# Kernel tuning notes

Measured on AMD Instinct MI355X. Metric: run time of the kernel, lower is better.

The kernel has to match this reference:

```python
import jax, jax.numpy as jnp
import numpy as np

N = 50000
F_IN = 256
F_OUT = 256
K = 5
E = 1_600_000
SQRT_2PI = float(np.sqrt(2.0 * np.pi))
SQRT_2 = float(np.sqrt(2.0))


def _ex_relu(mu, sigma):
    # expected value of relu(Normal(mu, sigma)) with sigma = variance
    is_zero = sigma == 0
    safe_sigma = jnp.where(is_zero, 1e-10, sigma)
    sqrt_sigma = jnp.sqrt(safe_sigma)
    w = mu / sqrt_sigma
    nr = sqrt_sigma * (jnp.exp(-0.5 * w * w) / SQRT_2PI
                       + 0.5 * w * (1.0 + jax.lax.erf(w / SQRT_2)))
    return jnp.where(is_zero, jnp.maximum(mu, 0.0), nr)


def _conv(h, src, dst):
    # SimpleConv(aggr='add', combine_root='self_loop'):
    # out[d] = h[d] + sum_{(s,d) in edges} h[s];  h: [K, N, O]
    agg = jnp.zeros_like(h).at[:, dst, :].add(h[:, src, :])
    return h + agg


def setup_inputs() -> dict:
    key = jax.random.key(0)
    ks = jax.random.split(key, 7)
    x = jax.random.normal(ks[0], (N, F_IN), dtype=jnp.float32)
    edges = jax.random.randint(ks[1], (2, E), 0, N, dtype=jnp.int64)
    mask = jax.random.randint(ks[2], (N, F_IN), 0, 2) == 1  # True = missing
    logp = jax.random.normal(ks[3], (K,), dtype=jnp.float32)
    means = jax.random.normal(ks[4], (K, F_IN), dtype=jnp.float32)
    logvars = jax.random.normal(ks[5], (K, F_IN), dtype=jnp.float32)
    weight = jax.random.normal(ks[6], (F_IN, F_OUT), dtype=jnp.float32) * (1.414 / np.sqrt(F_IN + F_OUT) * np.sqrt(6.0))
    bias = jnp.zeros((F_OUT,), dtype=jnp.float32)
    return {"x": x, "edges": edges, "mask": mask, "logp": logp,
            "means": means, "logvars": logvars, "weight": weight, "bias": bias}


def reference(x, edges, mask, logp, means, logvars, weight, bias):
    src, dst = edges[0], edges[1]
    variances = jnp.exp(logvars)                                   # [K, F]
    m = mask[None, :, :]                                           # [1, N, F]
    mean_mat = jnp.where(m, means[:, None, :], x[None, :, :])      # [K, N, F]
    var_mat = jnp.where(m, variances[:, None, :], 0.0)             # [K, N, F]

    transform_x = jnp.einsum('knf,fo->kno', mean_mat, weight) + bias
    transform_covs = jnp.einsum('knf,fo->kno', var_mat, weight * weight)

    conv_x = _conv(transform_x, src, dst)                          # [K, N, O]
    conv_covs = _conv(transform_covs, src, dst)                    # [K, N, O]

    expected_x = _ex_relu(conv_x, conv_covs)                       # [K, N, O]

    # GMM responsibilities over components
    diff2 = (mean_mat - means[:, None, :]) ** 2 / variances[:, None, :]
    log_n = (-0.5 * jnp.sum(diff2, axis=2)
             - 0.5 * F_IN * np.log(2.0 * np.pi)
             - 0.5 * jnp.sum(logvars))                             # [K, N]
    gamma = jax.nn.softmax(logp[:, None] + log_n, axis=0)          # [K, N]

    return jnp.sum(expected_x * gamma[:, :, None], axis=0)         # [N, O]
```

## Files before the change

### kernel.cpp

```cpp
#include <hip/hip_runtime.h>
#include <math.h>

#define F 256
#define KMIX 5
#define RECB 640
#define GR 16
#define GS 3136

typedef __attribute__((ext_vector_type(8))) short bf16x8;
typedef __attribute__((ext_vector_type(4))) float f32x4;

__device__ __forceinline__ float bf2f(unsigned short u) {
  union { unsigned int i; float f; } v; v.i = ((unsigned int)u) << 16; return v.f;
}
__device__ __forceinline__ unsigned short f2bf(float f) {
  union { float f; unsigned int i; } v; v.f = f;
  unsigned int u = v.i;
  unsigned int r = (u + 0x7fffu + ((u >> 16) & 1u)) >> 16;
  return (unsigned short)r;
}

__device__ __forceinline__ f32x4 MFMA(bf16x8 a, bf16x8 b, f32x4 c) {
  return __builtin_amdgcn_mfma_f32_16x16x32_bf16(a, b, c, 0, 0, 0);
}

__device__ __forceinline__ float ex_relu_fast(float mu, float sig) {
  const float c1 = 1.2732395447f;
  const float c2 = 2.5464790895f;
  float t = mu * mu;
  float u = t + c1 * sig;
  float v = t + c2 * sig + 1e-20f;
  float r = __builtin_amdgcn_rsqf(v);
  return 0.5f * mu + 0.5f * u * r;
}

__global__ void kzero(unsigned int* p, long long n) {
  long long i = (long long)blockIdx.x * blockDim.x + threadIdx.x;
  long long stride = (long long)gridDim.x * blockDim.x;
  for (; i < n; i += stride) p[i] = 0u;
}

__global__ __launch_bounds__(256) void k_tab(const float* __restrict__ logvars,
                                             float* __restrict__ ivar) {
  int i = blockIdx.x * 256 + threadIdx.x;
  if (i < KMIX * F) ivar[i] = __expf(-logvars[i]);
}

__global__ __launch_bounds__(256) void k_prep(
    const float* __restrict__ x, const int* __restrict__ mask,
    const float* __restrict__ logp, const float* __restrict__ means,
    const float* __restrict__ ivar,
    unsigned char* __restrict__ rec, float* __restrict__ gamma, int Npad) {
  int n = blockIdx.x;
  int f = threadIdx.x;
  int idx = n * F + f;
  float xv = x[idx];
  int m = mask[idx];
  unsigned char* rn = rec + (size_t)n * RECB;
  ((unsigned short*)rn)[f] = m ? (unsigned short)0 : f2bf(xv);
  int wave = threadIdx.x >> 6;
  int lane = threadIdx.x & 63;
  unsigned long long bal = __ballot(m != 0);
  if (lane == 0) *(unsigned long long*)(rn + 512 + wave * 8) = bal;
  float cb[KMIX];
#pragma unroll
  for (int k = 0; k < KMIX; ++k) {
    float d = xv - means[k * F + f];
    cb[k] = m ? 0.0f : d * d * ivar[k * F + f];
  }
  __shared__ float red[KMIX][4];
#pragma unroll
  for (int k = 0; k < KMIX; ++k) {
    float c = cb[k];
    for (int off = 32; off > 0; off >>= 1) c += __shfl_down(c, off, 64);
    if (lane == 0) red[k][wave] = c;
  }
  __syncthreads();
  if (threadIdx.x == 0) {
    float lg[KMIX], mx = -1e30f;
#pragma unroll
    for (int k = 0; k < KMIX; ++k) {
      float tot = red[k][0] + red[k][1] + red[k][2] + red[k][3];
      lg[k] = logp[k] - 0.5f * tot;
      mx = fmaxf(mx, lg[k]);
    }
    float den = 0.0f, e[KMIX];
#pragma unroll
    for (int k = 0; k < KMIX; ++k) { e[k] = __expf(lg[k] - mx); den += e[k]; }
    float inv = 1.0f / den;
#pragma unroll
    for (int k = 0; k < KMIX; ++k) gamma[k * Npad + n] = e[k] * inv;
  }
}

__global__ void k_count(const int* __restrict__ edges, int* __restrict__ cnt, int E) {
  int i = blockIdx.x * blockDim.x + threadIdx.x;
  if (i < E) {
    int dst = edges[E + i];
    int g = edges[i] / GS;
    atomicAdd(&cnt[dst * GR + g], 1);
  }
}

__global__ __launch_bounds__(1024) void k_scanA(const int* __restrict__ cnt,
                                                int* __restrict__ excl,
                                                int* __restrict__ bsum, int n) {
  __shared__ int s[1024];
  int t = threadIdx.x;
  int i = blockIdx.x * 1024 + t;
  int v = (i < n) ? cnt[i] : 0;
  s[t] = v;
  __syncthreads();
  for (int off = 1; off < 1024; off <<= 1) {
    int u = (t >= off) ? s[t - off] : 0;
    __syncthreads();
    s[t] += u;
    __syncthreads();
  }
  if (i < n) excl[i] = s[t] - v;
  if (t == 1023) bsum[blockIdx.x] = s[1023];
}

__global__ __launch_bounds__(1024) void k_scanB(int* __restrict__ bsum, int nb) {
  __shared__ int s[1024];
  int t = threadIdx.x;
  int v = (t < nb) ? bsum[t] : 0;
  s[t] = v;
  __syncthreads();
  for (int off = 1; off < 1024; off <<= 1) {
    int u = (t >= off) ? s[t - off] : 0;
    __syncthreads();
    s[t] += u;
    __syncthreads();
  }
  if (t < nb) bsum[t] = s[t] - v;
}

__global__ __launch_bounds__(1024) void k_scanC(int* __restrict__ offs,
                                                int* __restrict__ cur,
                                                const int* __restrict__ bsum,
                                                int n, int E) {
  int i = blockIdx.x * 1024 + threadIdx.x;
  if (i < n) {
    int v = offs[i] + bsum[blockIdx.x];
    offs[i] = v;
    cur[i] = v;
  }
  if (i == 0) offs[n] = E;
}

__global__ void k_fill(const int* __restrict__ edges, int* __restrict__ cur,
                       int* __restrict__ srclist, int E) {
  int i = blockIdx.x * blockDim.x + threadIdx.x;
  if (i < E) {
    int src = edges[i];
    int dst = edges[E + i];
    int g = src / GS;
    int pos = atomicAdd(&cur[dst * GR + g], 1);
    srclist[pos] = src;
  }
}

__global__ __launch_bounds__(1024) void k_gather(
    const unsigned char* __restrict__ rec,
    const int* __restrict__ offs, const int* __restrict__ srclist,
    unsigned short* __restrict__ xs_pack, unsigned short* __restrict__ sm_pack,
    float* __restrict__ degp1) {
  __shared__ float xs_l[16][257];
  __shared__ float sm_l[16][257];
  int tile = blockIdx.x;
  int wave = threadIdx.x >> 6, lane = threadIdx.x & 63;
  int fb = lane * 4;
  int n = tile * 16 + wave;
  const unsigned char* rn = rec + (size_t)n * RECB;
  ushort4 xv = *(const ushort4*)(rn + lane * 8);
  unsigned int mw = *(const unsigned int*)(rn + 512 + ((lane >> 3) << 2));
  unsigned int nib = (mw >> ((lane & 7) * 4)) & 0xFu;
  unsigned int macc = (nib | (nib << 7) | (nib << 14) | (nib << 21)) & 0x01010101u;
  float a0 = bf2f(xv.x), a1 = bf2f(xv.y), a2 = bf2f(xv.z), a3 = bf2f(xv.w);
  int s0 = offs[n * GR], s1 = offs[n * GR + GR];
  int i = s0;
  for (; i + 4 <= s1; i += 4) {
    int sa = srclist[i], sb = srclist[i + 1], sc = srclist[i + 2], sd = srclist[i + 3];
    const unsigned char* ra = rec + (size_t)sa * RECB;
    const unsigned char* rb = rec + (size_t)sb * RECB;
    const unsigned char* rc = rec + (size_t)sc * RECB;
    const unsigned char* rd = rec + (size_t)sd * RECB;
    ushort4 va = *(const ushort4*)(ra + lane * 8);
    ushort4 vb = *(const ushort4*)(rb + lane * 8);
    ushort4 vc = *(const ushort4*)(rc + lane * 8);
    ushort4 vd = *(const ushort4*)(rd + lane * 8);
    unsigned int wa = *(const unsigned int*)(ra + 512 + ((lane >> 3) << 2));
    unsigned int wb = *(const unsigned int*)(rb + 512 + ((lane >> 3) << 2));
    unsigned int wc = *(const unsigned int*)(rc + 512 + ((lane >> 3) << 2));
    unsigned int wd = *(const unsigned int*)(rd + 512 + ((lane >> 3) << 2));
    a0 += bf2f(va.x) + bf2f(vb.x) + bf2f(vc.x) + bf2f(vd.x);
    a1 += bf2f(va.y) + bf2f(vb.y) + bf2f(vc.y) + bf2f(vd.y);
    a2 += bf2f(va.z) + bf2f(vb.z) + bf2f(vc.z) + bf2f(vd.z);
    a3 += bf2f(va.w) + bf2f(vb.w) + bf2f(vc.w) + bf2f(vd.w);
    unsigned int na = (wa >> ((lane & 7) * 4)) & 0xFu;
    unsigned int nb = (wb >> ((lane & 7) * 4)) & 0xFu;
    unsigned int nc = (wc >> ((lane & 7) * 4)) & 0xFu;
    unsigned int nd = (wd >> ((lane & 7) * 4)) & 0xFu;
    macc += (na | (na << 7) | (na << 14) | (na << 21)) & 0x01010101u;
    macc += (nb | (nb << 7) | (nb << 14) | (nb << 21)) & 0x01010101u;
    macc += (nc | (nc << 7) | (nc << 14) | (nc << 21)) & 0x01010101u;
    macc += (nd | (nd << 7) | (nd << 14) | (nd << 21)) & 0x01010101u;
  }
  for (; i < s1; ++i) {
    int s = srclist[i];
    const unsigned char* rs = rec + (size_t)s * RECB;
    ushort4 sv = *(const ushort4*)(rs + lane * 8);
    unsigned int ws = *(const unsigned int*)(rs + 512 + ((lane >> 3) << 2));
    a0 += bf2f(sv.x); a1 += bf2f(sv.y); a2 += bf2f(sv.z); a3 += bf2f(sv.w);
    unsigned int ns = (ws >> ((lane & 7) * 4)) & 0xFu;
    macc += (ns | (ns << 7) | (ns << 14) | (ns << 21)) & 0x01010101u;
  }
  xs_l[wave][fb] = a0; xs_l[wave][fb + 1] = a1; xs_l[wave][fb + 2] = a2; xs_l[wave][fb + 3] = a3;
  sm_l[wave][fb] = (float)(macc & 0xFFu);
  sm_l[wave][fb + 1] = (float)((macc >> 8) & 0xFFu);
  sm_l[wave][fb + 2] = (float)((macc >> 16) & 0xFFu);
  sm_l[wave][fb + 3] = (float)(macc >> 24);
  if (lane == 0) degp1[n] = (float)(s1 - s0 + 1);
  __syncthreads();
  if (threadIdx.x < 512) {
    int slot = threadIdx.x;
    int kt = slot >> 6, l = slot & 63;
    int r = l & 15, q = l >> 4;
    int fbase = kt * 32 + q * 8;
    bf16x8 vx, vs;
#pragma unroll
    for (int j = 0; j < 8; ++j) {
      vx[j] = (short)f2bf(xs_l[r][fbase + j]);
      vs[j] = (short)f2bf(sm_l[r][fbase + j]);
    }
    long long po = ((long long)tile * 8 + kt) * 64 + l;
    ((bf16x8*)xs_pack)[po] = vx;
    ((bf16x8*)sm_pack)[po] = vs;
  }
}

__global__ __launch_bounds__(64) void k_bpack(
    const float* __restrict__ weight, const float* __restrict__ means,
    const float* __restrict__ logvars, unsigned short* __restrict__ bpack) {
  int bid = blockIdx.x;
  int kt = bid & 7, ot = (bid >> 3) & 15, m = bid >> 7;
  int l = threadIdx.x;
  int r = l & 15, q = l >> 4;
  int o = ot * 16 + r;
  bf16x8 v;
#pragma unroll
  for (int j = 0; j < 8; ++j) {
    int f = kt * 32 + q * 8 + j;
    float wv = weight[f * F + o];
    float val;
    if (m == 0) val = wv;
    else if (m <= 5) val = means[(m - 1) * F + f] * wv;
    else val = __expf(logvars[(m - 6) * F + f]) * wv * wv;
    v[j] = (short)f2bf(val);
  }
  ((bf16x8*)bpack)[((long long)(m * 16 + ot) * 8 + kt) * 64 + l] = v;
}

__global__ __launch_bounds__(256, 3) void k_gemm(
    const unsigned short* __restrict__ xs_pack, const unsigned short* __restrict__ sm_pack,
    const unsigned short* __restrict__ bpack, const float* __restrict__ degp1,
    const float* __restrict__ gamma, const float* __restrict__ bias,
    float* __restrict__ out, int N, int Npad, int RB) {
  int L = blockIdx.x;
  int rb = (L >> 5) * 8 + (L & 7);
  int bo = (L >> 3) & 3;
  if (rb >= RB) return;
  __shared__ unsigned char sp_lds[32768];
  int tid = threadIdx.x;
  int wave = tid >> 6, lane = tid & 63;
  int rw = wave >> 1, cw = wave & 1;
  int q = lane >> 4, r16 = lane & 15;
  int rt0 = rb * 4 + rw * 2;
  int ct0 = bo * 4 + cw * 2;
  const bf16x8* XP = (const bf16x8*)xs_pack;
  const bf16x8* BP = (const bf16x8*)bpack;

  {
    const uint4* src = (const uint4*)((const unsigned char*)sm_pack + (size_t)rb * 32768) + tid;
    uint4* dst = (uint4*)(void*)sp_lds + tid;
#pragma unroll
    for (int it = 0; it < 8; ++it) dst[it * 256] = src[it * 256];
  }

  f32x4 C1[2][2];
#pragma unroll
  for (int rt = 0; rt < 2; ++rt)
#pragma unroll
    for (int cc = 0; cc < 2; ++cc) C1[rt][cc] = (f32x4){0.f, 0.f, 0.f, 0.f};
#pragma unroll
  for (int kt = 0; kt < 8; ++kt) {
    bf16x8 a0 = XP[((size_t)rt0 * 8 + kt) * 64 + lane];
    bf16x8 a1 = XP[((size_t)(rt0 + 1) * 8 + kt) * 64 + lane];
#pragma unroll
    for (int cc = 0; cc < 2; ++cc) {
      bf16x8 b = BP[((size_t)(ct0 + cc) * 8 + kt) * 64 + lane];
      C1[0][cc] = MFMA(a0, b, C1[0][cc]);
      C1[1][cc] = MFMA(a1, b, C1[1][cc]);
    }
  }

  int row0 = rb * 64 + rw * 32 + q * 4;
  float dp[2][4];
#pragma unroll
  for (int rt = 0; rt < 2; ++rt)
#pragma unroll
    for (int rr = 0; rr < 4; ++rr) dp[rt][rr] = degp1[row0 + rt * 16 + rr];
  float bs[2];
#pragma unroll
  for (int cc = 0; cc < 2; ++cc) bs[cc] = bias[bo * 64 + cw * 32 + cc * 16 + r16];

  f32x4 outa[2][2];
#pragma unroll
  for (int rt = 0; rt < 2; ++rt)
#pragma unroll
    for (int cc = 0; cc < 2; ++cc) outa[rt][cc] = (f32x4){0.f, 0.f, 0.f, 0.f};

  __syncthreads();
  const unsigned char* myl = sp_lds + rw * 16384;

  for (int k = 0; k < KMIX; ++k) {
    float gm[2][4];
#pragma unroll
    for (int rt = 0; rt < 2; ++rt)
#pragma unroll
      for (int rr = 0; rr < 4; ++rr) gm[rt][rr] = gamma[k * Npad + row0 + rt * 16 + rr];
    f32x4 ax[2][2], ac[2][2];
#pragma unroll
    for (int rt = 0; rt < 2; ++rt)
#pragma unroll
      for (int cc = 0; cc < 2; ++cc) {
        ax[rt][cc] = C1[rt][cc];
        ac[rt][cc] = (f32x4){0.f, 0.f, 0.f, 0.f};
      }
#pragma unroll
    for (int kt = 0; kt < 8; ++kt) {
      bf16x8 sp0 = *(const bf16x8*)(myl + kt * 1024 + lane * 16);
      bf16x8 sp1 = *(const bf16x8*)(myl + 8192 + kt * 1024 + lane * 16);
#pragma unroll
      for (int cc = 0; cc < 2; ++cc) {
        int c = ct0 + cc;
        bf16x8 bw = BP[(((size_t)(1 + k) * 16 + c) * 8 + kt) * 64 + lane];
        bf16x8 bv = BP[(((size_t)(6 + k) * 16 + c) * 8 + kt) * 64 + lane];
        ax[0][cc] = MFMA(sp0, bw, ax[0][cc]);
        ax[1][cc] = MFMA(sp1, bw, ax[1][cc]);
        ac[0][cc] = MFMA(sp0, bv, ac[0][cc]);
        ac[1][cc] = MFMA(sp1, bv, ac[1][cc]);
      }
    }
#pragma unroll
    for (int rt = 0; rt < 2; ++rt)
#pragma unroll
      for (int cc = 0; cc < 2; ++cc)
#pragma unroll
        for (int rr = 0; rr < 4; ++rr) {
          float mu = ax[rt][cc][rr] + dp[rt][rr] * bs[cc];
          float e = ex_relu_fast(mu, ac[rt][cc][rr]);
          outa[rt][cc][rr] += gm[rt][rr] * e;
        }
  }

#pragma unroll
  for (int rt = 0; rt < 2; ++rt)
#pragma unroll
    for (int cc = 0; cc < 2; ++cc) {
      int col = bo * 64 + cw * 32 + cc * 16 + r16;
#pragma unroll
      for (int rr = 0; rr < 4; ++rr) {
        int row = row0 + rt * 16 + rr;
        if (row < N) out[(long long)row * F + col] = outa[rt][cc][rr];
      }
    }
}

extern "C" void kernel_launch(void* const* d_in, const int* in_sizes, int n_in,
                              void* d_out, int out_size, void* d_ws, size_t ws_size,
                              hipStream_t stream) {
  const float* x = (const float*)d_in[0];
  const int* edges = (const int*)d_in[1];
  const int* mask = (const int*)d_in[2];
  const float* logp = (const float*)d_in[3];
  const float* means = (const float*)d_in[4];
  const float* logvars = (const float*)d_in[5];
  const float* weight = (const float*)d_in[6];
  const float* bias = (const float*)d_in[7];
  float* out = (float*)d_out;

  int N = in_sizes[0] / F;
  int E = in_sizes[1] / 2;
  int Npad = ((N + 127) / 128) * 128;
  int RB = Npad / 64;
  int NB = N * GR;
  int SB = (NB + 1023) / 1024;

  char* w = (char*)d_ws;
  auto alloc = [&](size_t bytes) {
    char* p = w;
    w += (bytes + 255) & ~(size_t)255;
    return p;
  };
  unsigned char* rec = (unsigned char*)alloc((size_t)N * RECB);
  unsigned short* xsp = (unsigned short*)alloc((size_t)Npad * F * 2);
  unsigned short* smp = (unsigned short*)alloc((size_t)Npad * F * 2);
  unsigned short* bpk = (unsigned short*)alloc((size_t)11 * F * F * 2);
  int* cnt = (int*)alloc((size_t)NB * 4);
  int* offs = (int*)alloc((size_t)(NB + 1) * 4);
  int* cur = (int*)alloc((size_t)NB * 4);
  int* bsum = (int*)alloc((size_t)1024 * 4);
  int* srclist = (int*)alloc((size_t)E * 4);
  float* degp1 = (float*)alloc((size_t)Npad * 4);
  float* gamma = (float*)alloc((size_t)KMIX * Npad * 4);
  float* ivar = (float*)alloc((size_t)KMIX * F * 4);

  kzero<<<782, 256, 0, stream>>>((unsigned int*)cnt, NB);
  k_tab<<<(KMIX * F + 255) / 256, 256, 0, stream>>>(logvars, ivar);
  k_prep<<<N, 256, 0, stream>>>(x, mask, logp, means, ivar, rec, gamma, Npad);
  k_count<<<(E + 255) / 256, 256, 0, stream>>>(edges, cnt, E);
  k_scanA<<<SB, 1024, 0, stream>>>(cnt, offs, bsum, NB);
  k_scanB<<<1, 1024, 0, stream>>>(bsum, SB);
  k_scanC<<<SB, 1024, 0, stream>>>(offs, cur, bsum, NB, E);
  k_fill<<<(E + 255) / 256, 256, 0, stream>>>(edges, cur, srclist, E);
  k_gather<<<N / 16, 1024, 0, stream>>>(rec, offs, srclist, xsp, smp, degp1);
  k_bpack<<<11 * 16 * 8, 64, 0, stream>>>(weight, means, logvars, bpk);
  int NGG = (RB + 7) / 8;
  k_gemm<<<NGG * 32, 256, 0, stream>>>(xsp, smp, bpk, degp1, gamma, bias, out, N, Npad, RB);
}
```

Baseline: 774.1 us.

## Interleave weight/variance B-packs and split column loop to raise GEMM occupancy

The packed B operand is re-laid out so that the mean-weight and variance-weight fragments for each mixture component sit adjacent, letting one address fetch both. The GEMM epilogue loop is restructured to iterate over the two column tiles outermost, which halves the live accumulator set, and launch bounds are raised from 3 to 4 blocks per SM to use the freed registers for occupancy. The cost is that each block now walks the shared-memory A fragments and the gamma values twice, once per column tile.

```diff
diff --git a/kernel.cpp b/kernel.cpp
--- a/kernel.cpp
+++ b/kernel.cpp
@@ -259,10 +259,18 @@
     else val = __expf(logvars[(m - 6) * F + f]) * wv * wv;
     v[j] = (short)f2bf(val);
   }
-  ((bf16x8*)bpack)[((long long)(m * 16 + ot) * 8 + kt) * 64 + l] = v;
-}
-
-__global__ __launch_bounds__(256, 3) void k_gemm(
+  size_t idx;
+  if (m == 0) {
+    idx = ((size_t)ot * 8 + kt) * 64 + l;
+  } else {
+    int s = (m <= 5) ? 0 : 1;
+    int k = (m <= 5) ? (m - 1) : (m - 6);
+    idx = 8192 + ((((size_t)k * 16 + ot) * 8 + kt) * 64 + l) * 2 + s;
+  }
+  ((bf16x8*)bpack)[idx] = v;
+}
+
+__global__ __launch_bounds__(256, 4) void k_gemm(
     const unsigned short* __restrict__ xs_pack, const unsigned short* __restrict__ sm_pack,
     const unsigned short* __restrict__ bpack, const float* __restrict__ degp1,
     const float* __restrict__ gamma, const float* __restrict__ bias,
@@ -277,9 +285,9 @@
   int rw = wave >> 1, cw = wave & 1;
   int q = lane >> 4, r16 = lane & 15;
   int rt0 = rb * 4 + rw * 2;
-  int ct0 = bo * 4 + cw * 2;
   const bf16x8* XP = (const bf16x8*)xs_pack;
   const bf16x8* BP = (const bf16x8*)bpack;
+  const bf16x8* BPp = BP + 8192;
 
   {
     const uint4* src = (const uint4*)((const unsigned char*)sm_pack + (size_t)rb * 32768) + tid;
@@ -299,7 +307,7 @@
     bf16x8 a1 = XP[((size_t)(rt0 + 1) * 8 + kt) * 64 + lane];
 #pragma unroll
     for (int cc = 0; cc < 2; ++cc) {
-      bf16x8 b = BP[((size_t)(ct0 + cc) * 8 + kt) * 64 + lane];
+      bf16x8 b = BP[((size_t)(bo * 4 + cw * 2 + cc) * 8 + kt) * 64 + lane];
       C1[0][cc] = MFMA(a0, b, C1[0][cc]);
       C1[1][cc] = MFMA(a1, b, C1[1][cc]);
     }
@@ -311,71 +319,61 @@
   for (int rt = 0; rt < 2; ++rt)
 #pragma unroll
     for (int rr = 0; rr < 4; ++rr) dp[rt][rr] = degp1[row0 + rt * 16 + rr];
-  float bs[2];
-#pragma unroll
-  for (int cc = 0; cc < 2; ++cc) bs[cc] = bias[bo * 64 + cw * 32 + cc * 16 + r16];
-
-  f32x4 outa[2][2];
-#pragma unroll
-  for (int rt = 0; rt < 2; ++rt)
-#pragma unroll
-    for (int cc = 0; cc < 2; ++cc) outa[rt][cc] = (f32x4){0.f, 0.f, 0.f, 0.f};
 
   __syncthreads();
   const unsigned char* myl = sp_lds + rw * 16384;
 
-  for (int k = 0; k < KMIX; ++k) {
-    float gm[2][4];
+#pragma unroll
+  for (int cc = 0; cc < 2; ++cc) {
+    int c = bo * 4 + cw * 2 + cc;
+    float bs = bias[c * 16 + r16];
+    f32x4 outa[2];
+#pragma unroll
+    for (int rt = 0; rt < 2; ++rt) outa[rt] = (f32x4){0.f, 0.f, 0.f, 0.f};
+
+    for (int k = 0; k < KMIX; ++k) {
+      float gm[2][4];
+#pragma unroll
+      for (int rt = 0; rt < 2; ++rt)
+#pragma unroll
+        for (int rr = 0; rr < 4; ++rr) gm[rt][rr] = gamma[k * Npad + row0 + rt * 16 + rr];
+      f32x4 ax[2], ac[2];
+#pragma unroll
+      for (int rt = 0; rt < 2; ++rt) {
+        ax[rt] = C1[rt][cc];
+        ac[rt] = (f32x4){0.f, 0.f, 0.f, 0.f};
+      }
+#pragma unroll
+      for (int kt = 0; kt < 8; ++kt) {
+        bf16x8 sp0 = *(const bf16x8*)(myl + kt * 1024 + lane * 16);
+        bf16x8 sp1 = *(const bf16x8*)(myl + 8192 + kt * 1024 + lane * 16);
+        const bf16x8* pp = &BPp[((((size_t)k * 16 + c) * 8 + kt) * 64 + lane) * 2];
+        bf16x8 bw = pp[0];
+        bf16x8 bv = pp[1];
+        ax[0] = MFMA(sp0, bw, ax[0]);
+        ax[1] = MFMA(sp1, bw, ax[1]);
+        ac[0] = MFMA(sp0, bv, ac[0]);
+        ac[1] = MFMA(sp1, bv, ac[1]);
+      }
+#pragma unroll
+      for (int rt = 0; rt < 2; ++rt)
+#pragma unroll
+        for (int rr = 0; rr < 4; ++rr) {
+          float mu = ax[rt][rr] + dp[rt][rr] * bs;
+          float e = ex_relu_fast(mu, ac[rt][rr]);
+          outa[rt][rr] += gm[rt][rr] * e;
+        }
+    }
+
+    int col = c * 16 + r16;
 #pragma unroll
     for (int rt = 0; rt < 2; ++rt)
-#pragma unroll
-      for (int rr = 0; rr < 4; ++rr) gm[rt][rr] = gamma[k * Npad + row0 + rt * 16 + rr];
-    f32x4 ax[2][2], ac[2][2];
-#pragma unroll
-    for (int rt = 0; rt < 2; ++rt)
-#pragma unroll
-      for (int cc = 0; cc < 2; ++cc) {
-        ax[rt][cc] = C1[rt][cc];
-        ac[rt][cc] = (f32x4){0.f, 0.f, 0.f, 0.f};
-      }
-#pragma unroll
-    for (int kt = 0; kt < 8; ++kt) {
-      bf16x8 sp0 = *(const bf16x8*)(myl + kt * 1024 + lane * 16);
-      bf16x8 sp1 = *(const bf16x8*)(myl + 8192 + kt * 1024 + lane * 16);
-#pragma unroll
-      for (int cc = 0; cc < 2; ++cc) {
-        int c = ct0 + cc;
-        bf16x8 bw = BP[(((size_t)(1 + k) * 16 + c) * 8 + kt) * 64 + lane];
-        bf16x8 bv = BP[(((size_t)(6 + k) * 16 + c) * 8 + kt) * 64 + lane];
-        ax[0][cc] = MFMA(sp0, bw, ax[0][cc]);
-        ax[1][cc] = MFMA(sp1, bw, ax[1][cc]);
-        ac[0][cc] = MFMA(sp0, bv, ac[0][cc]);
-        ac[1][cc] = MFMA(sp1, bv, ac[1][cc]);
-      }
-    }
-#pragma unroll
-    for (int rt = 0; rt < 2; ++rt)
-#pragma unroll
-      for (int cc = 0; cc < 2; ++cc)
-#pragma unroll
-        for (int rr = 0; rr < 4; ++rr) {
-          float mu = ax[rt][cc][rr] + dp[rt][rr] * bs[cc];
-          float e = ex_relu_fast(mu, ac[rt][cc][rr]);
-          outa[rt][cc][rr] += gm[rt][rr] * e;
-        }
-  }
-
-#pragma unroll
-  for (int rt = 0; rt < 2; ++rt)
-#pragma unroll
-    for (int cc = 0; cc < 2; ++cc) {
-      int col = bo * 64 + cw * 32 + cc * 16 + r16;
 #pragma unroll
       for (int rr = 0; rr < 4; ++rr) {
         int row = row0 + rt * 16 + rr;
-        if (row < N) out[(long long)row * F + col] = outa[rt][cc][rr];
+        if (row < N) out[(long long)row * F + col] = outa[rt][rr];
       }
-    }
+  }
 }
 
 extern "C" void kernel_launch(void* const* d_in, const int* in_sizes, int n_in,
```

Result: slower. 843.4 us (+8.9%).
